# Performance work log

Measured on AMD Instinct MI355X. Metric: run time of the kernel, lower is better.

Reference implementation:

```python
import jax, jax.numpy as jnp
import numpy as np

B, S, T = 64, 256, 32
VS, VT = 4000, 32000
E = H = 512
L = 2
PAD_IDX = 1
BOS_IDX = 2


def setup_inputs() -> dict:
    key = jax.random.key(0)
    ks = jax.random.split(key, 16)
    u = lambda k, sh: jax.random.uniform(k, sh, jnp.float32, -0.08, 0.08)
    inp = {
        'X': jax.random.randint(ks[0], (B, S), 0, VS),
        'y': jax.random.randint(ks[1], (B, T), 0, VT),
        'emb_src': u(ks[2], (VS, E)).at[PAD_IDX].set(0.0),
        'emb_tgt': u(ks[3], (VT, E)).at[PAD_IDX].set(0.0),
        'enc_Wih': u(ks[4], (L, 4 * H, E)),
        'enc_Whh': u(ks[5], (L, 4 * H, H)),
        'enc_bih': u(ks[6], (L, 4 * H)),
        'enc_bhh': u(ks[7], (L, 4 * H)),
        'dec_Wih': u(ks[8], (L, 4 * H, E)),
        'dec_Whh': u(ks[9], (L, 4 * H, H)),
        'dec_bih': u(ks[10], (L, 4 * H)),
        'dec_bhh': u(ks[11], (L, 4 * H)),
        'fcW': u(ks[12], (VT, H)),
        'fcb': u(ks[13], (VT,)),
    }
    return inp


def _cell(x, h, c, Wih, Whh, bih, bhh):
    # PyTorch LSTM cell, gate order i,f,g,o. x:[B,E], h,c:[B,H]
    gates = x @ Wih.T + h @ Whh.T + bih + bhh  # [B,4H]
    i, f, g, o = jnp.split(gates, 4, axis=-1)
    c = jax.nn.sigmoid(f) * c + jax.nn.sigmoid(i) * jnp.tanh(g)
    h = jax.nn.sigmoid(o) * jnp.tanh(c)
    return h, c


def _stack_step(x, hs, cs, Wih, Whh, bih, bhh):
    # run num_layers stacked cells for one timestep; hs,cs: [L,B,H]
    new_h, new_c = [], []
    inp = x
    for l in range(Wih.shape[0]):
        h, c = _cell(inp, hs[l], cs[l], Wih[l], Whh[l], bih[l], bhh[l])
        new_h.append(h)
        new_c.append(c)
        inp = h
    return jnp.stack(new_h), jnp.stack(new_c), inp


def _forward(X, y, emb_src, emb_tgt, enc_Wih, enc_Whh, enc_bih, enc_bhh,
             dec_Wih, dec_Whh, dec_bih, dec_bhh, fcW, fcb):
    b = X.shape[0]
    # ----- encoder: LSTM over full (un-padded) source sequence -----
    xs = emb_src[X].transpose(1, 0, 2)  # [S,B,E] time-major
    h0 = jnp.zeros((L, b, H), xs.dtype)
    c0 = jnp.zeros((L, b, H), xs.dtype)

    def enc_step(carry, x):
        hs, cs = carry
        hs, cs, _ = _stack_step(x, hs, cs, enc_Wih, enc_Whh, enc_bih, enc_bhh)
        return (hs, cs), None

    (hs, cs), _ = jax.lax.scan(enc_step, (h0, c0), xs)

    bos = jnp.full((b, 1), BOS_IDX, y.dtype)
    dec_in = jnp.concatenate([bos, y[:, :-1]], axis=1)  # [B,T]
    toks = dec_in.transpose(1, 0)  # [T,B]

    def dec_step(carry, tok):
        hs, cs = carry
        x = emb_tgt[tok]  # [B,E]
        hs, cs, top = _stack_step(x, hs, cs, dec_Wih, dec_Whh, dec_bih, dec_bhh)
        return (hs, cs), top

    (_, _), tops = jax.lax.scan(dec_step, (hs, cs), toks)  # tops: [T,B,H]
    # model returns only the last time step's log-softmax prediction
    logits = tops[-1] @ fcW.T + fcb  # [B,VT]
    return jax.nn.log_softmax(logits, axis=-1)


def reference(X, y, emb_src, emb_tgt, enc_Wih, enc_Whh, enc_bih, enc_bhh,
              dec_Wih, dec_Whh, dec_bih, dec_bhh, fcW, fcb):
    return _forward(X, y, emb_src, emb_tgt, enc_Wih, enc_Whh, enc_bih, enc_bhh,
                    dec_Wih, dec_Whh, dec_bih, dec_bhh, fcW, fcb)
```

## Files before the change

### kernel.cpp

```cpp
#include <hip/hip_runtime.h>

#define NB 256
#define NT 256

typedef __attribute__((ext_vector_type(8))) short short8;
typedef __attribute__((ext_vector_type(4))) float f32x4;
typedef __attribute__((ext_vector_type(2))) unsigned long long ull2;

constexpr int Bz = 64, Sz = 256, Tz = 32, Ez = 512, Hz = 512, G4 = 2048, VT = 32000;

__device__ __forceinline__ unsigned short f2b(float f) {
    unsigned u; __builtin_memcpy(&u, &f, 4);
    u = (u + 0x7fffu + ((u >> 16) & 1u)) >> 16;
    return (unsigned short)u;
}
__device__ __forceinline__ float sgm(float x) { return 1.0f / (1.0f + __expf(-x)); }
__device__ __forceinline__ float tnh(float x) { return 1.0f - 2.0f / (1.0f + __expf(2.0f * x)); }

__global__ __launch_bounds__(NT) void init_kernel(
    unsigned* __restrict__ hbuf_u32, float* __restrict__ row_sums,
    unsigned* __restrict__ bars)
{
    const int idx = blockIdx.x * NT + threadIdx.x;
#pragma unroll
    for (int i = 0; i < 4; ++i) hbuf_u32[idx * 4 + i] = 0u;
    if (blockIdx.x == 0) {
        bars[threadIdx.x] = 0u;
        if (threadIdx.x < 64) row_sums[threadIdx.x] = 0.0f;
    }
}

__global__ __launch_bounds__(NT, 2) void scan_kernel(
    const int* __restrict__ X, const int* __restrict__ Y,
    const float* __restrict__ emb_src, const float* __restrict__ emb_tgt,
    const float* __restrict__ eWih, const float* __restrict__ eWhh,
    const float* __restrict__ ebih, const float* __restrict__ ebhh,
    const float* __restrict__ dWih, const float* __restrict__ dWhh,
    const float* __restrict__ dbih, const float* __restrict__ dbhh,
    unsigned short* __restrict__ hbuf,
    unsigned* __restrict__ bars)
{
    __shared__ __align__(16) unsigned char smem[39168];
    unsigned short* xh_lds = (unsigned short*)smem;
    float* gates_lds = (float*)(smem + 32768);
    float* c_lds     = (float*)(smem + 37888);

    const int tid  = threadIdx.x;
    const int bid  = blockIdx.x;
    const int lay  = bid >> 7;
    const int bt   = (bid >> 5) & 3;
    const int ht   = bid & 31;
    const int wave = tid >> 6;
    const int lane = tid & 63;
    const int nl   = lane & 15;
    const int quad = lane >> 4;

    unsigned* bar_arrive = bars + bt * 64;
    unsigned* bar_flag   = bars + bt * 64 + 32;
    unsigned gen = 0;

    auto barrier = [&]() {
        ++gen;
        __syncthreads();
        if (tid == 0) {
            unsigned old = __hip_atomic_fetch_add(bar_arrive, 1u,
                               __ATOMIC_RELAXED, __HIP_MEMORY_SCOPE_AGENT);
            if (old == gen * 64u - 1u) {
                __hip_atomic_store(bar_flag, gen,
                                   __ATOMIC_RELAXED, __HIP_MEMORY_SCOPE_AGENT);
            } else {
                while (__hip_atomic_load(bar_flag,
                           __ATOMIC_RELAXED, __HIP_MEMORY_SCOPE_AGENT) < gen)
                    __builtin_amdgcn_s_sleep(1);
            }
        }
        __syncthreads();
    };

    for (int i = tid; i < 320; i += NT) c_lds[i] = 0.0f;
    __syncthreads();

    short8 wfrag[32];
    float bias_r = 0.0f;
    const int r = wave * 512 + ht * 16 + nl;

    auto load_w = [&](const float* Wih, const float* Whh,
                      const float* bih, const float* bhh) {
        const float* wi = Wih + (size_t)(lay * G4 + r) * 512;
        const float* wh = Whh + (size_t)(lay * G4 + r) * 512;
#pragma unroll
        for (int kc = 0; kc < 32; ++kc) {
            const int k0 = kc * 32 + quad * 8;
            const float* s = (k0 < 512) ? (wi + k0) : (wh + (k0 - 512));
            short8 v;
#pragma unroll
            for (int j = 0; j < 8; ++j) v[j] = (short)f2b(s[j]);
            wfrag[kc] = v;
        }
        bias_r = bih[lay * G4 + r] + bhh[lay * G4 + r];
    };

    const int kx = (nl >> 2) & 1;
    const int qx = quad ^ (nl & 3);

    auto step = [&](const float* xtab, const int* tk, const unsigned short* xb,
                    const unsigned short* hrow, unsigned short* hout) {
        const int rb = wave << 2;
        if (xtab) {
#pragma unroll
            for (int rr = 0; rr < 4; ++rr) {
                const int rw = rb + rr;
                const float* s = xtab + (size_t)tk[rr] * Ez + (lane << 3);
                float4 lo = *(const float4*)s;
                float4 hi = *(const float4*)(s + 4);
                short8 v;
                v[0] = (short)f2b(lo.x); v[1] = (short)f2b(lo.y);
                v[2] = (short)f2b(lo.z); v[3] = (short)f2b(lo.w);
                v[4] = (short)f2b(hi.x); v[5] = (short)f2b(hi.y);
                v[6] = (short)f2b(hi.z); v[7] = (short)f2b(hi.w);
                *(short8*)(xh_lds + (rw << 10) + ((lane ^ (rw & 7)) << 3)) = v;
            }
        } else {
#pragma unroll
            for (int rr = 0; rr < 4; ++rr) {
                const int rw = rb + rr;
                const unsigned long long* s =
                    (const unsigned long long*)(xb + ((size_t)(bt * 16 + rw) << 9)) + (lane << 1);
                unsigned long long a = __hip_atomic_load(s,
                        __ATOMIC_RELAXED, __HIP_MEMORY_SCOPE_AGENT);
                unsigned long long b = __hip_atomic_load(s + 1,
                        __ATOMIC_RELAXED, __HIP_MEMORY_SCOPE_AGENT);
                *(ull2*)(xh_lds + (rw << 10) + ((lane ^ (rw & 7)) << 3)) = (ull2){a, b};
            }
        }
#pragma unroll
        for (int rr = 0; rr < 4; ++rr) {
            const int rw = rb + rr;
            const unsigned long long* s =
                (const unsigned long long*)(hrow + ((size_t)(bt * 16 + rw) << 9)) + (lane << 1);
            unsigned long long a = __hip_atomic_load(s,
                    __ATOMIC_RELAXED, __HIP_MEMORY_SCOPE_AGENT);
            unsigned long long b = __hip_atomic_load(s + 1,
                    __ATOMIC_RELAXED, __HIP_MEMORY_SCOPE_AGENT);
            *(ull2*)(xh_lds + (rw << 10) + 512 + ((lane ^ (rw & 7)) << 3)) = (ull2){a, b};
        }
        __syncthreads();

        const unsigned short* arE = xh_lds + (nl << 10) + (qx << 3) + (kx << 5);
        const unsigned short* arO = xh_lds + (nl << 10) + (qx << 3) - (kx << 5);
        f32x4 a0 = {0.f, 0.f, 0.f, 0.f}, a1 = a0, a2 = a0, a3 = a0;
#pragma unroll
        for (int kc = 0; kc < 32; kc += 4) {
            short8 x0 = *(const short8*)(arE + ((kc + 0) << 5));
            short8 x1 = *(const short8*)(arO + ((kc + 1) << 5));
            short8 x2 = *(const short8*)(arE + ((kc + 2) << 5));
            short8 x3 = *(const short8*)(arO + ((kc + 3) << 5));
            a0 = __builtin_amdgcn_mfma_f32_16x16x32_bf16(x0, wfrag[kc + 0], a0, 0, 0, 0);
            a1 = __builtin_amdgcn_mfma_f32_16x16x32_bf16(x1, wfrag[kc + 1], a1, 0, 0, 0);
            a2 = __builtin_amdgcn_mfma_f32_16x16x32_bf16(x2, wfrag[kc + 2], a2, 0, 0, 0);
            a3 = __builtin_amdgcn_mfma_f32_16x16x32_bf16(x3, wfrag[kc + 3], a3, 0, 0, 0);
        }
        f32x4 acc = (a0 + a1) + (a2 + a3);
#pragma unroll
        for (int i = 0; i < 4; ++i) {
            float v = acc[i] + bias_r;
            v = (wave == 2) ? tnh(v) : sgm(v);
            gates_lds[wave * 320 + (quad * 4 + i) * 20 + nl] = v;
        }
        __syncthreads();
        if (tid < 128) {
            const int m = tid >> 3, np = tid & 7;
            float hp[2];
#pragma unroll
            for (int j = 0; j < 2; ++j) {
                const int n = 2 * np + j;
                const float iv = gates_lds[      m * 20 + n];
                const float fv = gates_lds[320 + m * 20 + n];
                const float gv = gates_lds[640 + m * 20 + n];
                const float ov = gates_lds[960 + m * 20 + n];
                float c = c_lds[m * 20 + n];
                c = fv * c + iv * gv;
                c_lds[m * 20 + n] = c;
                hp[j] = ov * tnh(c);
            }
            const unsigned pack = (unsigned)f2b(hp[0]) | ((unsigned)f2b(hp[1]) << 16);
            unsigned* dst = (unsigned*)&hout[(size_t)(bt * 16 + m) * 512 + ht * 16 + 2 * np];
            __hip_atomic_store(dst, pack, __ATOMIC_RELAXED, __HIP_MEMORY_SCOPE_AGENT);
        }
    };

    auto hb = [&](int l, int p) { return hbuf + (size_t)(l * 2 + p) * Bz * Hz; };

    load_w(eWih, eWhh, ebih, ebhh);
    for (int t = 0; t <= Sz; ++t) {
        if (lay == 0) {
            if (t < Sz) {
                int tk[4];
#pragma unroll
                for (int rr = 0; rr < 4; ++rr)
                    tk[rr] = X[(bt * 16 + (wave << 2) + rr) * Sz + t];
                step(emb_src, tk, nullptr, hb(0, (t + 1) & 1), hb(0, t & 1));
            }
        } else {
            if (t >= 1) {
                const int s = t - 1;
                step(nullptr, nullptr, hb(0, s & 1),
                     hb(1, (s + 1) & 1), hb(1, s & 1));
            }
        }
        barrier();
    }

    load_w(dWih, dWhh, dbih, dbhh);
    for (int t = 0; t <= Tz; ++t) {
        if (lay == 0) {
            if (t < Tz) {
                int tk[4];
#pragma unroll
                for (int rr = 0; rr < 4; ++rr)
                    tk[rr] = (t == 0) ? 2 : Y[(bt * 16 + (wave << 2) + rr) * Tz + t - 1];
                step(emb_tgt, tk, nullptr, hb(0, (t + 1) & 1), hb(0, t & 1));
            }
        } else {
            if (t >= 1) {
                const int s = t - 1;
                step(nullptr, nullptr, hb(0, s & 1),
                     hb(1, (s + 1) & 1), hb(1, s & 1));
            }
        }
        barrier();
    }
}

__global__ __launch_bounds__(NT, 1) void fc_kernel(
    const float* __restrict__ fcW, const float* __restrict__ fcb,
    const unsigned short* __restrict__ hbuf,
    float* __restrict__ logits, float* __restrict__ row_sums)
{
    __shared__ __align__(16) unsigned char smem[66816];
    unsigned short* h_lds = (unsigned short*)smem;
    float* row_part = (float*)(smem + 64 * 520 * 2);

    const int tid  = threadIdx.x;
    const int bid  = blockIdx.x;
    const int wave = tid >> 6;
    const int lane = tid & 63;
    const int nl   = lane & 15;
    const int quad = lane >> 4;

    {
        const unsigned short* htop = hbuf + (size_t)3 * Bz * Hz;
        const int rr2 = tid >> 2, pp = tid & 3;
        const short8* s = (const short8*)(htop + rr2 * 512 + pp * 128);
        short8* d = (short8*)(h_lds + rr2 * 520 + pp * 128);
#pragma unroll
        for (int i = 0; i < 16; ++i) d[i] = s[i];
    }
    if (tid < 64) row_part[tid] = 0.f;
    __syncthreads();

    const int c0 = bid * 128;
    f32x4 acc[8];
#pragma unroll
    for (int ct = 0; ct < 8; ++ct) acc[ct] = (f32x4){0.f, 0.f, 0.f, 0.f};
    const unsigned short* ar = h_lds + (wave * 16 + nl) * 520 + quad * 8;
    const float* bb = fcW + ((size_t)c0 + nl) * 512 + quad * 8;
    for (int kc = 0; kc < 16; ++kc) {
        short8 a = *(const short8*)(ar + kc * 32);
#pragma unroll
        for (int ct = 0; ct < 8; ++ct) {
            const float* bp = bb + (size_t)ct * 16 * 512 + kc * 32;
            float4 lo = *(const float4*)(bp);
            float4 hi = *(const float4*)(bp + 4);
            short8 b;
            b[0] = (short)f2b(lo.x); b[1] = (short)f2b(lo.y);
            b[2] = (short)f2b(lo.z); b[3] = (short)f2b(lo.w);
            b[4] = (short)f2b(hi.x); b[5] = (short)f2b(hi.y);
            b[6] = (short)f2b(hi.z); b[7] = (short)f2b(hi.w);
            acc[ct] = __builtin_amdgcn_mfma_f32_16x16x32_bf16(a, b, acc[ct], 0, 0, 0);
        }
    }
    float ls[4] = {0.f, 0.f, 0.f, 0.f};
#pragma unroll
    for (int ct = 0; ct < 8; ++ct) {
        const int col = c0 + ct * 16 + nl;
        const float bias = fcb[col];
#pragma unroll
        for (int i = 0; i < 4; ++i) {
            const float lg = acc[ct][i] + bias;
            logits[(size_t)(wave * 16 + quad * 4 + i) * VT + col] = lg;
            ls[i] += __expf(lg);
        }
    }
#pragma unroll
    for (int i = 0; i < 4; ++i)
        atomicAdd(&row_part[wave * 16 + quad * 4 + i], ls[i]);
    __syncthreads();
    if (tid < 64) atomicAdd(&row_sums[tid], row_part[tid]);
}

__global__ __launch_bounds__(NT) void norm_kernel(
    const float* __restrict__ logits, const float* __restrict__ row_sums,
    float* __restrict__ out)
{
    const int idx = blockIdx.x * NT + threadIdx.x;
    const int row = idx / VT;
    out[idx] = logits[idx] - __logf(row_sums[row]);
}

extern "C" void kernel_launch(void* const* d_in, const int* in_sizes, int n_in,
                              void* d_out, int out_size, void* d_ws, size_t ws_size,
                              hipStream_t stream) {
    const int* X = (const int*)d_in[0];
    const int* Y = (const int*)d_in[1];
    const float* emb_src = (const float*)d_in[2];
    const float* emb_tgt = (const float*)d_in[3];
    const float* eWih = (const float*)d_in[4];
    const float* eWhh = (const float*)d_in[5];
    const float* ebih = (const float*)d_in[6];
    const float* ebhh = (const float*)d_in[7];
    const float* dWih = (const float*)d_in[8];
    const float* dWhh = (const float*)d_in[9];
    const float* dbih = (const float*)d_in[10];
    const float* dbhh = (const float*)d_in[11];
    const float* fcW = (const float*)d_in[12];
    const float* fcb = (const float*)d_in[13];
    float* out = (float*)d_out;

    unsigned short* hbuf = (unsigned short*)d_ws;
    float* row_sums = (float*)((char*)d_ws + 262144);
    unsigned* bars  = (unsigned*)((char*)d_ws + 266240);
    float* logits   = (float*)((char*)d_ws + 524288);

    init_kernel<<<dim3(64), dim3(NT), 0, stream>>>((unsigned*)hbuf, row_sums, bars);

    void* args[] = {&X, &Y, &emb_src, &emb_tgt, &eWih, &eWhh, &ebih, &ebhh,
                    &dWih, &dWhh, &dbih, &dbhh, &hbuf, &bars};
    hipLaunchCooperativeKernel(reinterpret_cast<void*>(scan_kernel),
                               dim3(NB), dim3(NT), args, 0, stream);

    fc_kernel<<<dim3(VT / 128), dim3(NT), 0, stream>>>(fcW, fcb, hbuf, logits, row_sums);

    norm_kernel<<<dim3((Bz * VT) / NT), dim3(NT), 0, stream>>>(logits, row_sums, out);
}
```

Baseline: 1.626 ms.

## Prefetch next-step embeddings before grid barrier and overlap decoder weight load

Layer-0 blocks now gather and bf16-convert the next timestep's embedding rows into LDS right after the current step's MFMA/gate work, so the gather happens before the grid-wide barrier instead of on the critical path. Layer-0 blocks also load decoder weights during the idle final encoder iteration, while layer-1 blocks do it afterwards. The last redundant barrier of the decoder loop is dropped. This relies on the x-half of the LDS tile not being overwritten between the prestage and the next step, and it adds some register pressure.

```diff
diff --git a/kernel.cpp b/kernel.cpp
--- a/kernel.cpp
+++ b/kernel.cpp
@@ -103,36 +103,8 @@
     const int kx = (nl >> 2) & 1;
     const int qx = quad ^ (nl & 3);
 
-    auto step = [&](const float* xtab, const int* tk, const unsigned short* xb,
-                    const unsigned short* hrow, unsigned short* hout) {
+    auto stage_h = [&](const unsigned short* hrow) {
         const int rb = wave << 2;
-        if (xtab) {
-#pragma unroll
-            for (int rr = 0; rr < 4; ++rr) {
-                const int rw = rb + rr;
-                const float* s = xtab + (size_t)tk[rr] * Ez + (lane << 3);
-                float4 lo = *(const float4*)s;
-                float4 hi = *(const float4*)(s + 4);
-                short8 v;
-                v[0] = (short)f2b(lo.x); v[1] = (short)f2b(lo.y);
-                v[2] = (short)f2b(lo.z); v[3] = (short)f2b(lo.w);
-                v[4] = (short)f2b(hi.x); v[5] = (short)f2b(hi.y);
-                v[6] = (short)f2b(hi.z); v[7] = (short)f2b(hi.w);
-                *(short8*)(xh_lds + (rw << 10) + ((lane ^ (rw & 7)) << 3)) = v;
-            }
-        } else {
-#pragma unroll
-            for (int rr = 0; rr < 4; ++rr) {
-                const int rw = rb + rr;
-                const unsigned long long* s =
-                    (const unsigned long long*)(xb + ((size_t)(bt * 16 + rw) << 9)) + (lane << 1);
-                unsigned long long a = __hip_atomic_load(s,
-                        __ATOMIC_RELAXED, __HIP_MEMORY_SCOPE_AGENT);
-                unsigned long long b = __hip_atomic_load(s + 1,
-                        __ATOMIC_RELAXED, __HIP_MEMORY_SCOPE_AGENT);
-                *(ull2*)(xh_lds + (rw << 10) + ((lane ^ (rw & 7)) << 3)) = (ull2){a, b};
-            }
-        }
 #pragma unroll
         for (int rr = 0; rr < 4; ++rr) {
             const int rw = rb + rr;
@@ -144,8 +116,43 @@
                     __ATOMIC_RELAXED, __HIP_MEMORY_SCOPE_AGENT);
             *(ull2*)(xh_lds + (rw << 10) + 512 + ((lane ^ (rw & 7)) << 3)) = (ull2){a, b};
         }
-        __syncthreads();
-
+    };
+    auto stage_xb = [&](const unsigned short* xb) {
+        const int rb = wave << 2;
+#pragma unroll
+        for (int rr = 0; rr < 4; ++rr) {
+            const int rw = rb + rr;
+            const unsigned long long* s =
+                (const unsigned long long*)(xb + ((size_t)(bt * 16 + rw) << 9)) + (lane << 1);
+            unsigned long long a = __hip_atomic_load(s,
+                    __ATOMIC_RELAXED, __HIP_MEMORY_SCOPE_AGENT);
+            unsigned long long b = __hip_atomic_load(s + 1,
+                    __ATOMIC_RELAXED, __HIP_MEMORY_SCOPE_AGENT);
+            *(ull2*)(xh_lds + (rw << 10) + ((lane ^ (rw & 7)) << 3)) = (ull2){a, b};
+        }
+    };
+    auto prestage_x = [&](const float* xtab, const int* tok, int stride, int col, int bos) {
+        const int rb = wave << 2;
+        int tk[4];
+#pragma unroll
+        for (int rr = 0; rr < 4; ++rr)
+            tk[rr] = bos ? 2 : tok[(bt * 16 + rb + rr) * stride + col];
+#pragma unroll
+        for (int rr = 0; rr < 4; ++rr) {
+            const int rw = rb + rr;
+            const float* s = xtab + (size_t)tk[rr] * Ez + (lane << 3);
+            float4 lo = *(const float4*)s;
+            float4 hi = *(const float4*)(s + 4);
+            short8 v;
+            v[0] = (short)f2b(lo.x); v[1] = (short)f2b(lo.y);
+            v[2] = (short)f2b(lo.z); v[3] = (short)f2b(lo.w);
+            v[4] = (short)f2b(hi.x); v[5] = (short)f2b(hi.y);
+            v[6] = (short)f2b(hi.z); v[7] = (short)f2b(hi.w);
+            *(short8*)(xh_lds + (rw << 10) + ((lane ^ (rw & 7)) << 3)) = v;
+        }
+    };
+
+    auto mfma_tail = [&](unsigned short* hout) {
         const unsigned short* arE = xh_lds + (nl << 10) + (qx << 3) + (kx << 5);
         const unsigned short* arO = xh_lds + (nl << 10) + (qx << 3) - (kx << 5);
         f32x4 a0 = {0.f, 0.f, 0.f, 0.f}, a1 = a0, a2 = a0, a3 = a0;
@@ -192,43 +199,49 @@
     auto hb = [&](int l, int p) { return hbuf + (size_t)(l * 2 + p) * Bz * Hz; };
 
     load_w(eWih, eWhh, ebih, ebhh);
+    if (lay == 0) prestage_x(emb_src, X, Sz, 0, 0);
     for (int t = 0; t <= Sz; ++t) {
         if (lay == 0) {
             if (t < Sz) {
-                int tk[4];
-#pragma unroll
-                for (int rr = 0; rr < 4; ++rr)
-                    tk[rr] = X[(bt * 16 + (wave << 2) + rr) * Sz + t];
-                step(emb_src, tk, nullptr, hb(0, (t + 1) & 1), hb(0, t & 1));
+                stage_h(hb(0, (t + 1) & 1));
+                __syncthreads();
+                mfma_tail(hb(0, t & 1));
+                if (t + 1 < Sz) prestage_x(emb_src, X, Sz, t + 1, 0);
+                else            prestage_x(emb_tgt, nullptr, 0, 0, 1);
+            } else {
+                load_w(dWih, dWhh, dbih, dbhh);
             }
         } else {
             if (t >= 1) {
                 const int s = t - 1;
-                step(nullptr, nullptr, hb(0, s & 1),
-                     hb(1, (s + 1) & 1), hb(1, s & 1));
+                stage_xb(hb(0, s & 1));
+                stage_h(hb(1, (s + 1) & 1));
+                __syncthreads();
+                mfma_tail(hb(1, s & 1));
             }
         }
         barrier();
     }
 
-    load_w(dWih, dWhh, dbih, dbhh);
+    if (lay == 1) load_w(dWih, dWhh, dbih, dbhh);
     for (int t = 0; t <= Tz; ++t) {
         if (lay == 0) {
             if (t < Tz) {
-                int tk[4];
-#pragma unroll
-                for (int rr = 0; rr < 4; ++rr)
-                    tk[rr] = (t == 0) ? 2 : Y[(bt * 16 + (wave << 2) + rr) * Tz + t - 1];
-                step(emb_tgt, tk, nullptr, hb(0, (t + 1) & 1), hb(0, t & 1));
+                stage_h(hb(0, (t + 1) & 1));
+                __syncthreads();
+                mfma_tail(hb(0, t & 1));
+                if (t + 1 < Tz) prestage_x(emb_tgt, Y, Tz, t, 0);
             }
         } else {
             if (t >= 1) {
                 const int s = t - 1;
-                step(nullptr, nullptr, hb(0, s & 1),
-                     hb(1, (s + 1) & 1), hb(1, s & 1));
-            }
-        }
-        barrier();
+                stage_xb(hb(0, s & 1));
+                stage_h(hb(1, (s + 1) & 1));
+                __syncthreads();
+                mfma_tail(hb(1, s & 1));
+            }
+        }
+        if (t < Tz) barrier();
     }
 }
 
```

Result: slower. 1.664 ms (+2.3%).
